# Performance work log

Hardware: AMD Instinct MI355X
Metric: run time of the kernel (lower is better)

## Reference

```python
import jax, jax.numpy as jnp
import numpy as np

E = 8            # moe_num_experts
HIDDEN = 1024    # hidden_size
FFN = 4096       # ffn_hidden_size
TOKENS = 8192    # total tokens, pre-sorted by expert; balanced -> TOKENS // E per expert


def setup_inputs() -> dict:
    key = jax.random.key(0)
    k1, k2, k3 = jax.random.split(key, 3)
    x = jax.random.normal(k1, (TOKENS, HIDDEN), dtype=jnp.float32)
    # w1, w2 stored flattened as [E*FFN, HIDDEN], matching create_dmoe_expert_weights' view([-1, columns])
    w1 = jax.random.normal(k2, (E * FFN, HIDDEN), dtype=jnp.float32) * (1.0 / np.sqrt(HIDDEN))
    w2 = jax.random.normal(k3, (E * FFN, HIDDEN), dtype=jnp.float32) * (1.0 / np.sqrt(FFN))
    return {"x": x, "w1": w1, "w2": w2, "num_experts": E}


def reference(x, w1, w2, num_experts):
    # Block-diagonal topology of dMoE SparseMLP: tokens sorted by expert, each
    # expert owns a contiguous FFN slice of w1/w2. Equivalent grouped GEMM:
    #   out_e = gelu(x_e @ w1_e^T) @ w2_e   (megablocks gelu = tanh-approx GELU)
    tokens, hidden = x.shape
    ffn = w1.shape[0] // num_experts
    tpe = tokens // num_experts  # tokens per expert (balanced topology)
    xe = x.reshape(num_experts, tpe, hidden)        # [E, T/E, H]
    w1e = w1.reshape(num_experts, ffn, hidden)      # [E, F, H]
    w2e = w2.reshape(num_experts, ffn, hidden)      # [E, F, H]
    h = jax.nn.gelu(jnp.einsum('eth,efh->etf', xe, w1e), approximate=True)  # sdd + gelu
    out = jnp.einsum('etf,efh->eth', h, w2e)        # dsd
    return out.reshape(tokens, hidden)
```

## Files before the change

kernel.cpp:

```cpp
#include <hip/hip_runtime.h>
#include <hip/hip_bf16.h>
#include <stdint.h>

#define NE 8
#define HID 1024
#define FFN 4096
#define TOK 8192
#define TPE (TOK / NE)

typedef __attribute__((ext_vector_type(8))) short    bf16x8;
typedef __attribute__((ext_vector_type(4))) float    f32x4;
typedef __attribute__((ext_vector_type(4))) unsigned short ushort4v;
typedef __attribute__((ext_vector_type(8))) unsigned short ushort8v;


__device__ __forceinline__ unsigned short f2bf(float f) {
    union { float f; unsigned u; } c; c.f = f;
    unsigned r = c.u + 0x7fffu + ((c.u >> 16) & 1u);
    return (unsigned short)(r >> 16);
}

__device__ __forceinline__ float gelu_tanh(float x) {
    const float c0 = 0.7978845608028654f;
    const float c1 = 0.044715f;
    float u = c0 * (x + c1 * x * x * x);
    float t = 1.0f - 2.0f / (1.0f + __expf(2.0f * u));
    return 0.5f * x * (1.0f + t);
}

typedef const __attribute__((address_space(1))) void gbl_void_t;
typedef __attribute__((address_space(3))) void lds_void_t;

__device__ __forceinline__ void gload_lds16(const void* g, void* l) {
    __builtin_amdgcn_global_load_lds((gbl_void_t*)g, (lds_void_t*)l, 16, 0, 0);
}


__global__ void cvt_f32_bf16(const float* __restrict__ in,
                             unsigned short* __restrict__ out) {
    size_t i = ((size_t)blockIdx.x * blockDim.x + threadIdx.x) * 8;
    f32x4 a = *(const f32x4*)(in + i);
    f32x4 b = *(const f32x4*)(in + i + 4);
    ushort8v o;
#pragma unroll
    for (int j = 0; j < 4; j++) { o[j] = f2bf(a[j]); o[4 + j] = f2bf(b[j]); }
    *(ushort8v*)(out + i) = o;
}


__global__ void transpose_cvt(const float* __restrict__ in,
                              unsigned short* __restrict__ out) {
    __shared__ unsigned short tile[64][65];
    const int e  = blockIdx.z;
    const int f0 = blockIdx.x * 64;
    const int h0 = blockIdx.y * 64;
    const float*     src = in  + (size_t)e * FFN * HID;
    unsigned short*  dst = out + (size_t)e * HID * FFN;
    const int t  = threadIdx.x;
    const int tr = t >> 4;
    const int tc = (t & 15) * 4;
#pragma unroll
    for (int i = 0; i < 4; i++) {
        int f = i * 16 + tr;
        f32x4 v = *(const f32x4*)(src + (size_t)(f0 + f) * HID + h0 + tc);
#pragma unroll
        for (int j = 0; j < 4; j++) tile[f][tc + j] = f2bf(v[j]);
    }
    __syncthreads();
#pragma unroll
    for (int i = 0; i < 4; i++) {
        int h = i * 16 + tr;
        ushort4v o;
#pragma unroll
        for (int j = 0; j < 4; j++) o[j] = tile[tc + j][h];
        *(ushort4v*)(dst + (size_t)(h0 + h) * FFN + f0 + tc) = o;
    }
}


template <int BN, int GX, int GY, bool GELU>
__global__ __launch_bounds__(512, 2)
void gemm8p(const unsigned short* __restrict__ A,
            const unsigned short* __restrict__ B,
            void* __restrict__ Cout, int M, int N, int K) {
    constexpr int BM = 256, BK = 64;
    constexpr int NH = BN / 128;
    constexpr int NI = 2 * NH;
    constexpr int LB = BN / 128;
    constexpr int S  = BN / 8;
    constexpr int ABYTES = BM * BK * 2;
    constexpr int BBYTES = BN * BK * 2;
    constexpr int BUF = ABYTES + BBYTES;
    constexpr int VMC = 2 + 2 * LB;
    constexpr int NWG = NE * GX * GY;

    __shared__ __align__(16) char lds[2 * BUF];

    const int lin = blockIdx.x;
    const int wid = (lin & 7) * (NWG >> 3) + (lin >> 3);
    const int e   = wid / (GX * GY);
    const int rem = wid % (GX * GY);
    const int m0  = (rem % GX) * BM;
    const int n0  = (rem / GX) * BN;

    const size_t K2 = (size_t)K * 2;
    const char* Ae = (const char*)(A + (size_t)e * M * K);
    const char* Be = (const char*)(B + (size_t)e * N * K);

    const int tid  = threadIdx.x;
    const int lane = tid & 63;
    const int w    = tid >> 6;
    const int wr   = w >> 2, wc = w & 3;
    const int fr   = lane & 15, fq = lane >> 4;

    const int rA  = tid >> 3;
    const int kb  = (tid & 7) * 16;
    const int kbs = kb ^ ((rA & 7) << 4);
    const char* aptr = Ae + (size_t)(m0 + rA) * K2 + kbs;
    const int   fB   = (rA / S) * 2 * S + (rA % S);
    const char* bptr = Be + (size_t)(n0 + fB) * K2 + kbs;
    char* dA0 = lds + rA * 128 + kb;
    char* dA1 = dA0 + BUF;
    char* dB0 = lds + ABYTES + fB * 128 + kb;
    char* dB1 = dB0 + BUF;

    auto SA = [&](int au, int kt, char* d) {
        const char* s = aptr + (size_t)kt * 128;
#pragma unroll
        for (int i = 0; i < 2; i++)
            gload_lds16(s + (size_t)(au * 64 + i * 128) * K2,
                        d + (au * 64 + i * 128) * 128);
    };
    auto SB = [&](int bu, int kt, char* d) {
        const char* s = bptr + (size_t)kt * 128;
#pragma unroll
        for (int i = 0; i < LB; i++)
            gload_lds16(s + (size_t)(bu * S + i * 128) * K2,
                        d + (bu * S + i * 128) * 128);
    };

    const int kx0 = (fq * 16) ^ ((lane & 7) << 4);
    const char* paA = lds + (wr * 128 + fr) * 128;
    const char* paB = lds + ABYTES + (wc * (BN / 4) + fr) * 128;
    const char* pa0k0 = paA + kx0;        const char* pa0k1 = paA + (kx0 ^ 64);
    const char* pa1k0 = pa0k0 + BUF;      const char* pa1k1 = pa0k1 + BUF;
    const char* pb0k0 = paB + kx0;        const char* pb0k1 = paB + (kx0 ^ 64);
    const char* pb1k0 = pb0k0 + BUF;      const char* pb1k1 = pb0k1 + BUF;

    f32x4 acc[8][NI];
#pragma unroll
    for (int i = 0; i < 8; i++)
#pragma unroll
        for (int j = 0; j < NI; j++) acc[i][j] = f32x4{0.f, 0.f, 0.f, 0.f};

    bf16x8 a[4][2], b0[NH][2], b1[NH][2];

    auto LDA = [&](const char* p0, const char* p1, int mq) {
#pragma unroll
        for (int mi = 0; mi < 4; mi++) {
            a[mi][0] = *(const bf16x8*)(p0 + mq * 8192 + mi * 2048);
            a[mi][1] = *(const bf16x8*)(p1 + mq * 8192 + mi * 2048);
        }
    };
    auto LDB = [&](const char* p0, const char* p1, int nq, bf16x8 (&bb)[NH][2]) {
#pragma unroll
        for (int ni = 0; ni < NH; ni++) {
            bb[ni][0] = *(const bf16x8*)(p0 + (nq * (BN / 8) + ni * 16) * 128);
            bb[ni][1] = *(const bf16x8*)(p1 + (nq * (BN / 8) + ni * 16) * 128);
        }
    };
    auto MMQ = [&](int mq, int nq, bf16x8 (&bb)[NH][2]) {
        __builtin_amdgcn_s_setprio(1);
#pragma unroll
        for (int mi = 0; mi < 4; mi++)
#pragma unroll
            for (int ni = 0; ni < NH; ni++) {
                f32x4& c = acc[mq * 4 + mi][nq * NH + ni];
                c = __builtin_amdgcn_mfma_f32_16x16x32_bf16(a[mi][0], bb[ni][0], c, 0, 0, 0);
                c = __builtin_amdgcn_mfma_f32_16x16x32_bf16(a[mi][1], bb[ni][1], c, 0, 0, 0);
            }
        __builtin_amdgcn_s_setprio(0);
    };

#define MIDBAR()  __builtin_amdgcn_s_barrier();                                      \
                  asm volatile("s_waitcnt lgkmcnt(0)" ::: "memory");                 \
                  __builtin_amdgcn_sched_barrier(0)
#define ENDBAR()  __builtin_amdgcn_s_barrier();                                      \
                  __builtin_amdgcn_sched_barrier(0)
#define LGHINT()  asm volatile("s_waitcnt lgkmcnt(8)" ::: "memory")
#define VMW()     asm volatile("s_waitcnt vmcnt(%0)" :: "n"(VMC) : "memory")

    const int NT   = K / BK;
    const int NTm1 = NT - 1;

    SA(0, 0, dA0); SB(0, 0, dB0); SB(1, 0, dB0); SA(1, 0, dA0);
    SA(0, 1, dA1); SB(0, 1, dB1); SB(1, 1, dB1);
    VMW();
    __builtin_amdgcn_s_barrier();
    __builtin_amdgcn_sched_barrier(0);

    const int NW = NT / 2;
    for (int ww = 0; ww < NW; ++ww) {
        const int T = 2 * ww;
        const int kt1 = T + 1;
        const int kt2 = (T + 2 < NT) ? T + 2 : NTm1;
        const int kt3 = (T + 3 < NT) ? T + 3 : NTm1;

        LDA(pa0k0, pa0k1, 0); LDB(pb0k0, pb0k1, 0, b0); SA(1, kt1, dA1);
        LGHINT(); MIDBAR(); MMQ(0, 0, b0); ENDBAR();
        LDB(pb0k0, pb0k1, 1, b1); SA(0, kt2, dA0);
        MIDBAR(); MMQ(0, 1, b1); ENDBAR();
        LDA(pa0k0, pa0k1, 1); SB(0, kt2, dB0);
        MIDBAR(); MMQ(1, 1, b1); ENDBAR();
        SB(1, kt2, dB0);
        MIDBAR(); MMQ(1, 0, b0); VMW(); ENDBAR();
        LDA(pa1k0, pa1k1, 0); LDB(pb1k0, pb1k1, 0, b0); SA(1, kt2, dA0);
        LGHINT(); MIDBAR(); MMQ(0, 0, b0); ENDBAR();
        LDB(pb1k0, pb1k1, 1, b1); SA(0, kt3, dA1);
        MIDBAR(); MMQ(0, 1, b1); ENDBAR();
        LDA(pa1k0, pa1k1, 1); SB(0, kt3, dB1);
        MIDBAR(); MMQ(1, 1, b1); ENDBAR();
        SB(1, kt3, dB1);
        MIDBAR(); MMQ(1, 0, b0); VMW(); ENDBAR();
    }
    asm volatile("s_waitcnt vmcnt(0)" ::: "memory");

    const int r0 = m0 + wr * 128 + fq * 4;
    const int c0 = n0 + wc * (BN / 4) + fr;
    if constexpr (GELU) {
        unsigned short* C = (unsigned short*)Cout + (size_t)e * M * N;
#pragma unroll
        for (int mi = 0; mi < 8; mi++)
#pragma unroll
            for (int ni = 0; ni < NI; ni++) {
                int row = r0 + mi * 16, col = c0 + ni * 16;
#pragma unroll
                for (int r = 0; r < 4; r++)
                    C[(size_t)(row + r) * N + col] = f2bf(gelu_tanh(acc[mi][ni][r]));
            }
    } else {
        float* C = (float*)Cout + (size_t)e * M * N;
#pragma unroll
        for (int mi = 0; mi < 8; mi++)
#pragma unroll
            for (int ni = 0; ni < NI; ni++) {
                int row = r0 + mi * 16, col = c0 + ni * 16;
#pragma unroll
                for (int r = 0; r < 4; r++)
                    C[(size_t)(row + r) * N + col] = acc[mi][ni][r];
            }
    }
#undef MIDBAR
#undef ENDBAR
#undef LGHINT
#undef VMW
}


__global__ void fused_fallback(const float* __restrict__ x,
                               const float* __restrict__ w1,
                               const float* __restrict__ w2,
                               float* __restrict__ out) {
    __shared__ float xs[HID];
    __shared__ float hs[FFN];
    const int tok = blockIdx.x;
    const int e   = tok / TPE;
    const float* w1e = w1 + (size_t)e * FFN * HID;
    const float* w2e = w2 + (size_t)e * FFN * HID;
    const int t = threadIdx.x;
    for (int i = t; i < HID; i += 256) xs[i] = x[(size_t)tok * HID + i];
    __syncthreads();
    for (int f = t; f < FFN; f += 256) {
        const float* wr_ = w1e + (size_t)f * HID;
        float s = 0.f;
        for (int k = 0; k < HID; k++) s += xs[k] * wr_[k];
        hs[f] = gelu_tanh(s);
    }
    __syncthreads();
    for (int h = t; h < HID; h += 256) {
        float s = 0.f;
        for (int f = 0; f < FFN; f++) s += hs[f] * w2e[(size_t)f * HID + h];
        out[(size_t)tok * HID + h] = s;
    }
}


extern "C" void kernel_launch(void* const* d_in, const int* in_sizes, int n_in,
                              void* d_out, int out_size, void* d_ws, size_t ws_size,
                              hipStream_t stream) {
    const float* x  = (const float*)d_in[0];
    const float* w1 = (const float*)d_in[1];
    const float* w2 = (const float*)d_in[2];
    float* out = (float*)d_out;

    const size_t XB  = (size_t)TOK * HID * 2;
    const size_t W1B = (size_t)NE * FFN * HID * 2;
    const size_t W2B = W1B;
    const size_t HB  = (size_t)TOK * FFN * 2;
    const size_t need = XB + W1B + W2B + HB;

    if (ws_size >= need) {
        char* ws = (char*)d_ws;
        unsigned short* xb  = (unsigned short*)ws;
        unsigned short* w1b = (unsigned short*)(ws + XB);
        unsigned short* w2t = (unsigned short*)(ws + XB + W1B);
        unsigned short* hb  = (unsigned short*)(ws + XB + W1B + W2B);

        cvt_f32_bf16<<<(TOK * HID) / (256 * 8), 256, 0, stream>>>(x, xb);
        cvt_f32_bf16<<<(NE * FFN * HID) / (256 * 8), 256, 0, stream>>>(w1, w1b);
        transpose_cvt<<<dim3(FFN / 64, HID / 64, NE), 256, 0, stream>>>(w2, w2t);

        gemm8p<256, TPE / 256, FFN / 256, true><<<NE * (TPE / 256) * (FFN / 256), 512, 0, stream>>>(
            xb, w1b, hb, TPE, FFN, HID);
        gemm8p<128, TPE / 256, HID / 128, false><<<NE * (TPE / 256) * (HID / 128), 512, 0, stream>>>(
            hb, w2t, out, TPE, HID, FFN);
    } else {
        fused_fallback<<<TOK, 256, 0, stream>>>(x, w1, w2, out);
    }
}
```

Baseline: 237.5 us.

## Merge conversion kernels into one launch and reorder GEMM pipeline stages

The three preprocessing kernels (x cast, w1 cast, w2 transpose-cast) are merged into one launch that dispatches on block index, which removes two launch gaps and lets the three jobs overlap. Separately, the GEMM main loop moves LDS reads to before the end barrier of the previous MFMA phase and groups the B stores, aiming to overlap LDS reads with MFMA work. The merged kernel raises LDS use for the cast blocks, and the reordered schedule could change hazard or occupancy behavior.

```diff
diff --git a/kernel.cpp b/kernel.cpp
--- a/kernel.cpp
+++ b/kernel.cpp
@@ -36,26 +36,34 @@
 }
 
 
-__global__ void cvt_f32_bf16(const float* __restrict__ in,
-                             unsigned short* __restrict__ out) {
-    size_t i = ((size_t)blockIdx.x * blockDim.x + threadIdx.x) * 8;
-    f32x4 a = *(const f32x4*)(in + i);
-    f32x4 b = *(const f32x4*)(in + i + 4);
-    ushort8v o;
-#pragma unroll
-    for (int j = 0; j < 4; j++) { o[j] = f2bf(a[j]); o[4 + j] = f2bf(b[j]); }
-    *(ushort8v*)(out + i) = o;
-}
-
-
-__global__ void transpose_cvt(const float* __restrict__ in,
-                              unsigned short* __restrict__ out) {
+#define XBLKS  ((TOK * HID) / 2048)
+#define W1BLKS ((NE * FFN * HID) / 2048)
+#define TBLKS  (NE * (FFN / 64) * (HID / 64))
+
+__global__ void prep_all(const float* __restrict__ x,  unsigned short* __restrict__ xb,
+                         const float* __restrict__ w1, unsigned short* __restrict__ w1b,
+                         const float* __restrict__ w2, unsigned short* __restrict__ w2t) {
     __shared__ unsigned short tile[64][65];
-    const int e  = blockIdx.z;
-    const int f0 = blockIdx.x * 64;
-    const int h0 = blockIdx.y * 64;
-    const float*     src = in  + (size_t)e * FFN * HID;
-    unsigned short*  dst = out + (size_t)e * HID * FFN;
+    int bid = blockIdx.x;
+    if (bid < XBLKS + W1BLKS) {
+        const float* in; unsigned short* out; size_t i;
+        if (bid < XBLKS) { in = x;  out = xb;  i = ((size_t)bid * 256 + threadIdx.x) * 8; }
+        else             { in = w1; out = w1b; i = ((size_t)(bid - XBLKS) * 256 + threadIdx.x) * 8; }
+        f32x4 a = *(const f32x4*)(in + i);
+        f32x4 b = *(const f32x4*)(in + i + 4);
+        ushort8v o;
+#pragma unroll
+        for (int j = 0; j < 4; j++) { o[j] = f2bf(a[j]); o[4 + j] = f2bf(b[j]); }
+        *(ushort8v*)(out + i) = o;
+        return;
+    }
+    bid -= XBLKS + W1BLKS;
+    const int e  = bid / ((FFN / 64) * (HID / 64));
+    const int r_ = bid % ((FFN / 64) * (HID / 64));
+    const int f0 = (r_ / (HID / 64)) * 64;
+    const int h0 = (r_ % (HID / 64)) * 64;
+    const float*     src = w2  + (size_t)e * FFN * HID;
+    unsigned short*  dst = w2t + (size_t)e * HID * FFN;
     const int t  = threadIdx.x;
     const int tr = t >> 4;
     const int tc = (t & 15) * 4;
@@ -207,20 +215,22 @@
         const int kt3 = (T + 3 < NT) ? T + 3 : NTm1;
 
         LDA(pa0k0, pa0k1, 0); LDB(pb0k0, pb0k1, 0, b0); SA(1, kt1, dA1);
-        LGHINT(); MIDBAR(); MMQ(0, 0, b0); ENDBAR();
-        LDB(pb0k0, pb0k1, 1, b1); SA(0, kt2, dA0);
-        MIDBAR(); MMQ(0, 1, b1); ENDBAR();
-        LDA(pa0k0, pa0k1, 1); SB(0, kt2, dB0);
+        LGHINT(); MIDBAR(); MMQ(0, 0, b0);
+        LDB(pb0k0, pb0k1, 1, b1); ENDBAR();
+        SA(0, kt2, dA0);
+        MIDBAR(); MMQ(0, 1, b1);
+        LDA(pa0k0, pa0k1, 1); ENDBAR();
+        SB(0, kt2, dB0); SB(1, kt2, dB0);
         MIDBAR(); MMQ(1, 1, b1); ENDBAR();
-        SB(1, kt2, dB0);
         MIDBAR(); MMQ(1, 0, b0); VMW(); ENDBAR();
         LDA(pa1k0, pa1k1, 0); LDB(pb1k0, pb1k1, 0, b0); SA(1, kt2, dA0);
-        LGHINT(); MIDBAR(); MMQ(0, 0, b0); ENDBAR();
-        LDB(pb1k0, pb1k1, 1, b1); SA(0, kt3, dA1);
-        MIDBAR(); MMQ(0, 1, b1); ENDBAR();
-        LDA(pa1k0, pa1k1, 1); SB(0, kt3, dB1);
+        LGHINT(); MIDBAR(); MMQ(0, 0, b0);
+        LDB(pb1k0, pb1k1, 1, b1); ENDBAR();
+        SA(0, kt3, dA1);
+        MIDBAR(); MMQ(0, 1, b1);
+        LDA(pa1k0, pa1k1, 1); ENDBAR();
+        SB(0, kt3, dB1); SB(1, kt3, dB1);
         MIDBAR(); MMQ(1, 1, b1); ENDBAR();
-        SB(1, kt3, dB1);
         MIDBAR(); MMQ(1, 0, b0); VMW(); ENDBAR();
     }
     asm volatile("s_waitcnt vmcnt(0)" ::: "memory");
@@ -306,9 +316,7 @@
         unsigned short* w2t = (unsigned short*)(ws + XB + W1B);
         unsigned short* hb  = (unsigned short*)(ws + XB + W1B + W2B);
 
-        cvt_f32_bf16<<<(TOK * HID) / (256 * 8), 256, 0, stream>>>(x, xb);
-        cvt_f32_bf16<<<(NE * FFN * HID) / (256 * 8), 256, 0, stream>>>(w1, w1b);
-        transpose_cvt<<<dim3(FFN / 64, HID / 64, NE), 256, 0, stream>>>(w2, w2t);
+        prep_all<<<XBLKS + W1BLKS + TBLKS, 256, 0, stream>>>(x, xb, w1, w1b, w2, w2t);
 
         gemm8p<256, TPE / 256, FFN / 256, true><<<NE * (TPE / 256) * (FFN / 256), 512, 0, stream>>>(
             xb, w1b, hb, TPE, FFN, HID);
```

Result: faster. 232.4 us (-2.2%).
